# Optimization experiments

Measured on AMD Instinct MI355X. Metric: run time of the kernel, lower is better.

## Reference

```python
import jax, jax.numpy as jnp
import numpy as np

B, CH, T = 8, 512, 1024
HEADS = 8
KC = CH // HEADS  # 64
BLOCK = 256       # block_length


def setup_inputs() -> dict:
    key = jax.random.key(0)
    ks = jax.random.split(key, 10)
    s = 0.05
    x = jax.random.normal(ks[0], (B, CH, T), jnp.float32)
    c = jax.random.normal(ks[1], (B, CH, T), jnp.float32)
    attn_mask = jnp.ones((1, 1, T, T), jnp.int32)
    # 1x1 Conv1d weights are just [out, in] matrices over the channel dim.
    Wq = jax.random.normal(ks[2], (CH, CH), jnp.float32) * s
    bq = jax.random.normal(ks[3], (CH,), jnp.float32) * s
    Wk = jax.random.normal(ks[4], (CH, CH), jnp.float32) * s
    bk = jax.random.normal(ks[5], (CH,), jnp.float32) * s
    Wv = jax.random.normal(ks[6], (CH, CH), jnp.float32) * s
    bv = jax.random.normal(ks[7], (CH,), jnp.float32) * s
    Wo = jax.random.normal(ks[8], (CH, CH), jnp.float32) * s
    bo = jax.random.normal(ks[9], (CH,), jnp.float32) * s
    return {"x": x, "c": c, "attn_mask": attn_mask,
            "Wq": Wq, "bq": bq, "Wk": Wk, "bk": bk,
            "Wv": Wv, "bv": bv, "Wo": Wo, "bo": bo}


def _proj(W, b, z):
    # 1x1 Conv1d: [B,C,T] -> [B,O,T]
    return jnp.einsum('oc,bct->bot', W, z) + b[None, :, None]


def reference(x, c, attn_mask, Wq, bq, Wk, bk, Wv, bv, Wo, bo):
    q = _proj(Wq, bq, x)
    k = _proj(Wk, bk, c)
    v = _proj(Wv, bv, c)

    def split_heads(z):  # [B,C,T] -> [B,H,T,KC]
        return z.reshape(B, HEADS, KC, T).transpose(0, 1, 3, 2)

    qh, kh, vh = split_heads(q), split_heads(k), split_heads(v)

    scale = jnp.asarray(1.0 / np.sqrt(KC), qh.dtype)
    scores = jnp.einsum('bhtd,bhsd->bhts', qh * scale, kh)  # [B,H,T,T]

    r = jnp.arange(T)
    diff = jnp.abs(r[None, :] - r[:, None])  # |i - j|, [T,T]
    # proximal bias: -log(1 + |i-j|)
    scores = scores + (-jnp.log1p(diff.astype(scores.dtype)))[None, None]
    # attention mask: masked_fill(mask == 0, -1e4)
    scores = jnp.where(attn_mask == 0, jnp.asarray(-1e4, scores.dtype), scores)
    # block-length band mask: keep |i-j| <= BLOCK (triu(-BLOCK).tril(BLOCK))
    band = (diff <= BLOCK)[None, None]
    scores = jnp.where(band, scores, jnp.asarray(-1e4, scores.dtype))

    p_attn = jax.nn.softmax(scores, axis=-1)
    out = jnp.einsum('bhts,bhsd->bhtd', p_attn, vh)  # [B,H,T,KC]
    out = out.transpose(0, 1, 3, 2).reshape(B, CH, T)  # merge heads -> [B,C,T]
    return _proj(Wo, bo, out)
```

## Files before the change

kernel.cpp:

```cpp
#include <hip/hip_runtime.h>
#include <stdint.h>

typedef unsigned short u16;
typedef __attribute__((ext_vector_type(8))) __bf16 bf16x8;
typedef __attribute__((ext_vector_type(4))) float f32x4;

constexpr int B_ = 8, CH = 512, T = 1024, NH = 8, HD = 64, BAND = 256;

__device__ inline u16 f2b(float f) {
  union { float f; uint32_t u; } v; v.f = f;
  uint32_t r = (v.u + 0x7fffu + ((v.u >> 16) & 1u)) >> 16;
  return (u16)r;
}

__device__ inline f32x4 mfma16(bf16x8 a, bf16x8 b, f32x4 c) {
  return __builtin_amdgcn_mfma_f32_16x16x32_bf16(a, b, c, 0, 0, 0);
}

__device__ __forceinline__ void gld16(const void* g, void* l) {
  __builtin_amdgcn_global_load_lds((__attribute__((address_space(1))) void*)(g),
                                   (__attribute__((address_space(3))) void*)(l),
                                   16, 0, 0);
}

__device__ __forceinline__ float exp2_hw(float x) { return __builtin_amdgcn_exp2f(x); }

__global__ __launch_bounds__(256) void cvt_w(const float* __restrict__ wq, const float* __restrict__ wk,
                                             const float* __restrict__ wv, const float* __restrict__ wo,
                                             u16* __restrict__ out) {
  int idx = blockIdx.x * 256 + threadIdx.x;
  int w = idx >> 15;
  const float* src = (w == 0) ? wq : (w == 1) ? wk : (w == 2) ? wv : wo;
  int e = (idx & 32767) * 8;
  f32x4 a = *(const f32x4*)(src + e);
  f32x4 b = *(const f32x4*)(src + e + 4);
  union { u16 h[8]; bf16x8 v; } r;
  r.h[0] = f2b(a[0]); r.h[1] = f2b(a[1]); r.h[2] = f2b(a[2]); r.h[3] = f2b(a[3]);
  r.h[4] = f2b(b[0]); r.h[5] = f2b(b[1]); r.h[6] = f2b(b[2]); r.h[7] = f2b(b[3]);
  *(bf16x8*)(out + (w << 18) + e) = r.v;
}

__global__ __launch_bounds__(256) void tr_cvt(const float* __restrict__ x, const float* __restrict__ c,
                                              u16* __restrict__ xT, u16* __restrict__ cT) {
  __shared__ float tile[32][33];
  int z = blockIdx.z;
  const float* src = (z < B_) ? x : c;
  u16* dst = (z < B_) ? xT : cT;
  int b = (z < B_) ? z : z - B_;
  int t0 = blockIdx.x * 32, c0 = blockIdx.y * 32;
  int tx = threadIdx.x & 31, ty = threadIdx.x >> 5;
#pragma unroll
  for (int k = 0; k < 4; k++)
    tile[ty + 8 * k][tx] = src[(long)(b * CH + c0 + ty + 8 * k) * T + t0 + tx];
  __syncthreads();
#pragma unroll
  for (int k = 0; k < 4; k++)
    dst[(long)(b * T + t0 + ty + 8 * k) * CH + c0 + tx] = f2b(tile[tx][ty + 8 * k]);
}

template <int TN, typename OT>
__device__ __forceinline__ void gemm_core(const u16* __restrict__ Ab, int lda,
                                          const u16* __restrict__ Bb, int ldb,
                                          OT* __restrict__ Cb, int ldc,
                                          const float* __restrict__ bi, bool brow,
                                          int m0, int n0, int K, u16* smA, u16* smB) {
  int t = threadIdx.x, lane = t & 63, wave = t >> 6;
  int cl = lane & 15, quad = lane >> 4;
  int wm = wave >> 1, wn = wave & 1;
  int rr = t >> 3, gs = t & 7;
  constexpr int NW = TN / 32;
  f32x4 acc[4][NW] = {};
  for (int k0 = 0; k0 < K; k0 += 64) {
    __syncthreads();
#pragma unroll
    for (int j = 0; j < 4; j++) {
      int R = j * 32 + rr;
      int gc = (gs ^ (R & 7)) << 3;
      gld16(Ab + (long)(m0 + R) * lda + k0 + gc, (char*)smA + j * 4096 + wave * 1024);
      if (j < TN / 32)
        gld16(Bb + (long)(n0 + R) * ldb + k0 + gc, (char*)smB + j * 4096 + wave * 1024);
    }
    __syncthreads();
#pragma unroll
    for (int ks = 0; ks < 2; ks++) {
      int g2 = ((ks << 2) | quad) ^ (cl & 7);
      bf16x8 af[4], bb[NW];
#pragma unroll
      for (int i = 0; i < 4; i++)
        af[i] = *(const bf16x8*)&smA[(wm * 64 + i * 16 + cl) * 64 + g2 * 8];
#pragma unroll
      for (int i = 0; i < NW; i++)
        bb[i] = *(const bf16x8*)&smB[(wn * (TN / 2) + i * 16 + cl) * 64 + g2 * 8];
#pragma unroll
      for (int mi = 0; mi < 4; mi++)
#pragma unroll
        for (int ni = 0; ni < NW; ni++)
          acc[mi][ni] = mfma16(af[mi], bb[ni], acc[mi][ni]);
    }
  }
#pragma unroll
  for (int mi = 0; mi < 4; mi++) {
    int row = m0 + wm * 64 + mi * 16 + quad * 4;
#pragma unroll
    for (int ni = 0; ni < NW; ni++) {
      int col = n0 + wn * (TN / 2) + ni * 16 + cl;
#pragma unroll
      for (int r = 0; r < 4; r++) {
        float v = acc[mi][ni][r] + (brow ? bi[row + r] : bi[col]);
        if constexpr (sizeof(OT) == 2) Cb[(long)(row + r) * ldc + col] = f2b(v);
        else Cb[(long)(row + r) * ldc + col] = v;
      }
    }
  }
}

__global__ __launch_bounds__(256, 3) void gemm_qkv(const u16* __restrict__ xT, const u16* __restrict__ cT,
                                                   const u16* __restrict__ Wb,
                                                   u16* __restrict__ Qb, u16* __restrict__ Kb, u16* __restrict__ Vb,
                                                   const float* __restrict__ bq, const float* __restrict__ bk,
                                                   const float* __restrict__ bv) {
  __shared__ u16 smA[128 * 64], smB[128 * 64];
  const long TCH = (long)T * CH;
  int z = blockIdx.z, sec = z >> 3, zz = z & 7, bx = blockIdx.x;
  const u16 *Ab, *Bb; u16* Cb; const float* bi;
  int m0, n0, ldc; bool brow;
  if (sec == 0) {
    Ab = xT + zz * TCH; Bb = Wb;           Cb = Qb + zz * TCH;        bi = bq;
    m0 = (bx >> 2) * 128; n0 = (bx & 3) * 128; ldc = CH; brow = false;
  } else if (sec == 1) {
    Ab = cT + zz * TCH; Bb = Wb + 262144;  Cb = Kb + zz * TCH;        bi = bk;
    m0 = (bx >> 2) * 128; n0 = (bx & 3) * 128; ldc = CH; brow = false;
  } else {
    Ab = Wb + 2 * 262144; Bb = cT + zz * TCH; Cb = Vb + zz * (long)CH * T; bi = bv;
    m0 = (bx & 3) * 128; n0 = (bx >> 2) * 128; ldc = T; brow = true;
  }
  gemm_core<128, u16>(Ab, CH, Bb, CH, Cb, ldc, bi, brow, m0, n0, CH, smA, smB);
}

__global__ __launch_bounds__(256, 4) void gemm_o(const u16* __restrict__ Wo, const u16* __restrict__ AO,
                                                 float* __restrict__ out, const float* __restrict__ bo) {
  __shared__ u16 smA[128 * 64], smB[64 * 64];
  int z = blockIdx.z;
  gemm_core<64, float>(Wo, CH, AO + z * (long)T * CH, CH, out + z * (long)CH * T, T,
                       bo, true, blockIdx.y * 128, blockIdx.x * 64, CH, smA, smB);
}

__global__ __launch_bounds__(256, 3) void attn(const u16* __restrict__ Q, const u16* __restrict__ Kt,
                                               const u16* __restrict__ V, u16* __restrict__ AO) {
  __shared__ u16 sK[2][64 * 64];
  __shared__ u16 sV[2][64 * 64];
  __shared__ u16 sP[4][16 * 72];
  int lane = threadIdx.x & 63, wave = threadIdx.x >> 6;
  int cl = lane & 15, quad = lane >> 4;
  int bx = blockIdx.x;
  int xcd = bx & 7, ii = bx >> 3;
  int bh = xcd * 8 + (ii & 7);
  int qt = ii >> 3;
  int b = bh >> 3, h = bh & 7;
  int tq0 = qt * 64;
  int tqw = tq0 + wave * 16;
  const u16* qb = Q + ((long)(b * T + tqw + cl) * CH) + h * HD;
  bf16x8 qf0 = *(const bf16x8*)(qb + quad * 8);
  bf16x8 qf1 = *(const bf16x8*)(qb + 32 + quad * 8);
  f32x4 acc[4] = {};
  float lr[4] = {0.f, 0.f, 0.f, 0.f};
  float fir[4];
#pragma unroll
  for (int r = 0; r < 4; r++) fir[r] = (float)(tqw + quad * 4 + r);
  int lo = tq0 - BAND; if (lo < 0) lo = 0;
  int hi = tq0 + 64 + BAND; if (hi > T) hi = T;
  int nt = (hi - lo) >> 6;

  int rl = lane >> 3, cg = lane & 7;
  const u16* ksrc = Kt + (long)b * T * CH + h * HD;
  const u16* vsrc = V + ((long)(b * CH + h * HD) * T);

#define STAGE(buf, j0)                                                          \
  {                                                                             \
    _Pragma("unroll")                                                           \
    for (int i = 0; i < 2; i++) {                                               \
      int r = wave * 16 + i * 8 + rl;                                           \
      int s = ((r >> 5) << 5) + ((r >> 4) & 1) + ((r & 15) << 1);               \
      gld16(ksrc + (long)(j0 + s) * CH + ((cg ^ (r & 7)) << 3),                 \
            (char*)&sK[buf][(wave * 16 + i * 8) * 64]);                         \
      gld16(vsrc + (long)r * T + (j0) + ((cg ^ (r & 7)) << 3),                  \
            (char*)&sV[buf][(wave * 16 + i * 8) * 64]);                         \
    }                                                                           \
  }

  STAGE(0, lo)
  constexpr float C2 = 0.125f * 1.4426950408889634f;
  for (int it = 0; it < nt; it++) {
    int cur = it & 1;
    int j0 = lo + it * 64;
    __syncthreads();
    if (it + 1 < nt) STAGE(1 - cur, j0 + 64)
    f32x4 sg[2][2];
#pragma unroll
    for (int p = 0; p < 2; p++)
#pragma unroll
      for (int sub = 0; sub < 2; sub++) {
        const u16* kr = &sK[cur][(p * 32 + sub * 16 + cl) * 64];
        bf16x8 k0 = *(const bf16x8*)&kr[((quad ^ (cl & 7)) << 3)];
        bf16x8 k1 = *(const bf16x8*)&kr[(((4 | quad) ^ (cl & 7)) << 3)];
        f32x4 z = {0.f, 0.f, 0.f, 0.f};
        sg[p][sub] = mfma16(qf1, k1, mfma16(qf0, k0, z));
      }
#pragma unroll
    for (int p = 0; p < 2; p++) {
      float jb = (float)(j0 + p * 32 + 2 * cl);
#pragma unroll
      for (int r = 0; r < 4; r++) {
        float de = fabsf(fir[r] - jb);
        float dd = fabsf(fir[r] - jb - 1.f);
        float pe = exp2_hw(sg[p][0][r] * C2) * __builtin_amdgcn_rcpf(1.f + de);
        float po = exp2_hw(sg[p][1][r] * C2) * __builtin_amdgcn_rcpf(1.f + dd);
        pe = (de <= 256.f) ? pe : 0.f;
        po = (dd <= 256.f) ? po : 0.f;
        lr[r] += pe + po;
        uint32_t ue, uo;
        { union { float f; uint32_t u; } cv; cv.f = pe; ue = cv.u; cv.f = po; uo = cv.u; }
        uint32_t pk = ((uo + 0x8000u) & 0xffff0000u) | ((ue + 0x8000u) >> 16);
        *(uint32_t*)&sP[wave][(quad * 4 + r) * 72 + p * 32 + 2 * cl] = pk;
      }
    }
#pragma unroll
    for (int ks = 0; ks < 2; ks++) {
      bf16x8 pf = *(bf16x8*)&sP[wave][cl * 72 + ks * 32 + quad * 8];
#pragma unroll
      for (int dg = 0; dg < 4; dg++) {
        bf16x8 vf = *(const bf16x8*)&sV[cur][(dg * 16 + cl) * 64 +
                                             ((((ks << 2) | quad) ^ (cl & 7)) << 3)];
        acc[dg] = mfma16(pf, vf, acc[dg]);
      }
    }
  }
#undef STAGE
  float inv[4];
#pragma unroll
  for (int r = 0; r < 4; r++) {
    float s = lr[r];
    s += __shfl_xor(s, 1); s += __shfl_xor(s, 2);
    s += __shfl_xor(s, 4); s += __shfl_xor(s, 8);
    inv[r] = __builtin_amdgcn_rcpf(s);
  }
#pragma unroll
  for (int dg = 0; dg < 4; dg++)
#pragma unroll
    for (int r = 0; r < 4; r++)
      AO[((long)(b * T + tqw + quad * 4 + r) * CH) + h * HD + dg * 16 + cl] = f2b(acc[dg][r] * inv[r]);
}

extern "C" void kernel_launch(void* const* d_in, const int* in_sizes, int n_in,
                              void* d_out, int out_size, void* d_ws, size_t ws_size,
                              hipStream_t stream) {
  const float* x  = (const float*)d_in[0];
  const float* c  = (const float*)d_in[1];
  const float* Wq = (const float*)d_in[3];
  const float* bq = (const float*)d_in[4];
  const float* Wk = (const float*)d_in[5];
  const float* bk = (const float*)d_in[6];
  const float* Wv = (const float*)d_in[7];
  const float* bv = (const float*)d_in[8];
  const float* Wo = (const float*)d_in[9];
  const float* bo = (const float*)d_in[10];
  float* out = (float*)d_out;

  const long NT = (long)B_ * T * CH;
  u16* Wb = (u16*)d_ws;
  u16* xT = Wb + 4 * 262144;
  u16* cT = xT + NT;
  u16* Qb = cT + NT;
  u16* Kb = Qb + NT;
  u16* Vb = Kb + NT;
  u16* AO = xT;

  cvt_w<<<dim3(512), dim3(256), 0, stream>>>(Wq, Wk, Wv, Wo, Wb);
  tr_cvt<<<dim3(32, 16, 16), dim3(256), 0, stream>>>(x, c, xT, cT);
  gemm_qkv<<<dim3(32, 1, 24), dim3(256), 0, stream>>>(xT, cT, Wb, Qb, Kb, Vb, bq, bk, bv);
  attn<<<dim3(1024), dim3(256), 0, stream>>>(Qb, Kb, Vb, AO);
  gemm_o<<<dim3(16, 4, 8), dim3(256), 0, stream>>>(Wb + 3 * 262144, AO, out, bo);
}
```

Before: 156.6 us.

## Merge weight and input conversion kernels, swizzle P buffer, use packed bf16 convert

Folds the weight-conversion and transpose-conversion kernels into one prep launch that also uses 64x64 tiles with vectorized loads and 16-byte stores. In attention, the padded P scratch buffer becomes an XOR-swizzled 64-wide layout. The manual bf16 packing is replaced with the hardware v_cvt_pk_bf16_f32 instruction. The attention occupancy hint goes from 3 to 4 blocks per unit. Together these aim to cut launch overhead, global traffic inefficiency, LDS usage and ALU work, at the cost of possible register pressure from the higher occupancy target.

Result: faster. 151.9 us, median of 4 (-3.0%).

```diff
diff --git a/kernel.cpp b/kernel.cpp
--- a/kernel.cpp
+++ b/kernel.cpp
@@ -25,37 +25,51 @@
 
 __device__ __forceinline__ float exp2_hw(float x) { return __builtin_amdgcn_exp2f(x); }
 
-__global__ __launch_bounds__(256) void cvt_w(const float* __restrict__ wq, const float* __restrict__ wk,
-                                             const float* __restrict__ wv, const float* __restrict__ wo,
-                                             u16* __restrict__ out) {
-  int idx = blockIdx.x * 256 + threadIdx.x;
-  int w = idx >> 15;
-  const float* src = (w == 0) ? wq : (w == 1) ? wk : (w == 2) ? wv : wo;
-  int e = (idx & 32767) * 8;
-  f32x4 a = *(const f32x4*)(src + e);
-  f32x4 b = *(const f32x4*)(src + e + 4);
-  union { u16 h[8]; bf16x8 v; } r;
-  r.h[0] = f2b(a[0]); r.h[1] = f2b(a[1]); r.h[2] = f2b(a[2]); r.h[3] = f2b(a[3]);
-  r.h[4] = f2b(b[0]); r.h[5] = f2b(b[1]); r.h[6] = f2b(b[2]); r.h[7] = f2b(b[3]);
-  *(bf16x8*)(out + (w << 18) + e) = r.v;
-}
-
-__global__ __launch_bounds__(256) void tr_cvt(const float* __restrict__ x, const float* __restrict__ c,
-                                              u16* __restrict__ xT, u16* __restrict__ cT) {
-  __shared__ float tile[32][33];
-  int z = blockIdx.z;
-  const float* src = (z < B_) ? x : c;
-  u16* dst = (z < B_) ? xT : cT;
-  int b = (z < B_) ? z : z - B_;
-  int t0 = blockIdx.x * 32, c0 = blockIdx.y * 32;
-  int tx = threadIdx.x & 31, ty = threadIdx.x >> 5;
-#pragma unroll
-  for (int k = 0; k < 4; k++)
-    tile[ty + 8 * k][tx] = src[(long)(b * CH + c0 + ty + 8 * k) * T + t0 + tx];
+__global__ __launch_bounds__(256) void prep(const float* __restrict__ x, const float* __restrict__ c,
+                                            const float* __restrict__ wq, const float* __restrict__ wk,
+                                            const float* __restrict__ wv, const float* __restrict__ wo,
+                                            u16* __restrict__ xT, u16* __restrict__ cT, u16* __restrict__ Wb) {
+  int z = blockIdx.z, tid = threadIdx.x;
+  if (z == 16) {
+    int wb = blockIdx.y * 16 + blockIdx.x;
+    int w = wb >> 5;
+    const float* src = (w == 0) ? wq : (w == 1) ? wk : (w == 2) ? wv : wo;
+    int base = (wb & 31) * 8192;
+#pragma unroll
+    for (int i = 0; i < 4; i++) {
+      int e = base + i * 2048 + tid * 8;
+      f32x4 a = *(const f32x4*)(src + e);
+      f32x4 b = *(const f32x4*)(src + e + 4);
+      union { u16 h[8]; bf16x8 v; } r;
+      r.h[0] = f2b(a[0]); r.h[1] = f2b(a[1]); r.h[2] = f2b(a[2]); r.h[3] = f2b(a[3]);
+      r.h[4] = f2b(b[0]); r.h[5] = f2b(b[1]); r.h[6] = f2b(b[2]); r.h[7] = f2b(b[3]);
+      *(bf16x8*)(Wb + (w << 18) + e) = r.v;
+    }
+    return;
+  }
+  __shared__ float tile[64][65];
+  int b = z & 7;
+  const float* src = (z < 8) ? x : c;
+  u16* dst = (z < 8) ? xT : cT;
+  int t0 = blockIdx.x * 64, c0 = blockIdx.y * 64;
+  int t4 = (tid & 15) * 4, chb = tid >> 4;
+#pragma unroll
+  for (int p = 0; p < 4; p++) {
+    int ch = chb + p * 16;
+    f32x4 v = *(const f32x4*)(src + (long)(b * CH + c0 + ch) * T + t0 + t4);
+#pragma unroll
+    for (int j = 0; j < 4; j++) tile[t4 + j][ch] = v[j];
+  }
   __syncthreads();
-#pragma unroll
-  for (int k = 0; k < 4; k++)
-    dst[(long)(b * T + t0 + ty + 8 * k) * CH + c0 + tx] = f2b(tile[tx][ty + 8 * k]);
+  int o = tid & 7, trr = tid >> 3;
+#pragma unroll
+  for (int p = 0; p < 2; p++) {
+    int tr = trr + p * 32;
+    union { u16 h[8]; bf16x8 v; } r;
+#pragma unroll
+    for (int j = 0; j < 8; j++) r.h[j] = f2b(tile[tr][o * 8 + j]);
+    *(bf16x8*)(dst + (long)(b * T + t0 + tr) * CH + c0 + o * 8) = r.v;
+  }
 }
 
 template <int TN, typename OT>
@@ -145,11 +159,11 @@
                        bo, true, blockIdx.y * 128, blockIdx.x * 64, CH, smA, smB);
 }
 
-__global__ __launch_bounds__(256, 3) void attn(const u16* __restrict__ Q, const u16* __restrict__ Kt,
+__global__ __launch_bounds__(256, 4) void attn(const u16* __restrict__ Q, const u16* __restrict__ Kt,
                                                const u16* __restrict__ V, u16* __restrict__ AO) {
   __shared__ u16 sK[2][64 * 64];
   __shared__ u16 sV[2][64 * 64];
-  __shared__ u16 sP[4][16 * 72];
+  __shared__ u16 sP[4][16 * 64];
   int lane = threadIdx.x & 63, wave = threadIdx.x >> 6;
   int cl = lane & 15, quad = lane >> 4;
   int bx = blockIdx.x;
@@ -218,15 +232,16 @@
         pe = (de <= 256.f) ? pe : 0.f;
         po = (dd <= 256.f) ? po : 0.f;
         lr[r] += pe + po;
-        uint32_t ue, uo;
-        { union { float f; uint32_t u; } cv; cv.f = pe; ue = cv.u; cv.f = po; uo = cv.u; }
-        uint32_t pk = ((uo + 0x8000u) & 0xffff0000u) | ((ue + 0x8000u) >> 16);
-        *(uint32_t*)&sP[wave][(quad * 4 + r) * 72 + p * 32 + 2 * cl] = pk;
+        uint32_t pk;
+        asm("v_cvt_pk_bf16_f32 %0, %1, %2" : "=v"(pk) : "v"(pe), "v"(po));
+        int R = (quad << 2) | r;
+        *(uint32_t*)&sP[wave][(R << 6) + ((((p << 2) | (cl >> 2)) ^ (R & 7)) << 3) +
+                              ((cl & 3) << 1)] = pk;
       }
     }
 #pragma unroll
     for (int ks = 0; ks < 2; ks++) {
-      bf16x8 pf = *(bf16x8*)&sP[wave][cl * 72 + ks * 32 + quad * 8];
+      bf16x8 pf = *(bf16x8*)&sP[wave][(cl << 6) + ((((ks << 2) | quad) ^ (cl & 7)) << 3)];
 #pragma unroll
       for (int dg = 0; dg < 4; dg++) {
         bf16x8 vf = *(const bf16x8*)&sV[cur][(dg * 16 + cl) * 64 +
@@ -275,8 +290,7 @@
   u16* Vb = Kb + NT;
   u16* AO = xT;
 
-  cvt_w<<<dim3(512), dim3(256), 0, stream>>>(Wq, Wk, Wv, Wo, Wb);
-  tr_cvt<<<dim3(32, 16, 16), dim3(256), 0, stream>>>(x, c, xT, cT);
+  prep<<<dim3(16, 8, 17), dim3(256), 0, stream>>>(x, c, Wq, Wk, Wv, Wo, xT, cT, Wb);
   gemm_qkv<<<dim3(32, 1, 24), dim3(256), 0, stream>>>(xT, cT, Wb, Qb, Kb, Vb, bq, bk, bv);
   attn<<<dim3(1024), dim3(256), 0, stream>>>(Qb, Kb, Vb, AO);
   gemm_o<<<dim3(16, 4, 8), dim3(256), 0, stream>>>(Wb + 3 * 262144, AO, out, bo);
```
